# Kernel tuning notes

Hardware: AMD Instinct MI355X
Metric: run time of the kernel (lower is better)

The kernel has to match this reference:

```python
import jax, jax.numpy as jnp
import numpy as np

N, E = 50000, 1600000
IN_CH, OUT_CH = 256, 128
NUM_REL, NUM_BASES = 8, 4


def setup_inputs() -> dict:
    key = jax.random.key(0)
    ks = jax.random.split(key, 9)
    s = 0.05  # small init scale, mimics uniform(size, param)
    return {
        "x": jax.random.normal(ks[0], (N, IN_CH), dtype=jnp.float32),
        "edge_src": jax.random.randint(ks[1], (E,), 0, N, dtype=jnp.int32),
        "edge_dst": jax.random.randint(ks[2], (E,), 0, N, dtype=jnp.int32),
        "edge_type": jax.random.randint(ks[3], (E,), 0, NUM_REL, dtype=jnp.int32),
        "norm": jax.random.uniform(ks[4], (E,), dtype=jnp.float32),
        "basis": jax.random.normal(ks[5], (NUM_BASES, IN_CH, OUT_CH), dtype=jnp.float32) * s,
        "att": jax.random.normal(ks[6], (NUM_REL, NUM_BASES), dtype=jnp.float32) * s,
        "root": jax.random.normal(ks[7], (IN_CH, OUT_CH), dtype=jnp.float32) * s,
        "bias": jax.random.normal(ks[8], (OUT_CH,), dtype=jnp.float32) * s,
    }


def reference(x, edge_src, edge_dst, edge_type, norm, basis, att, root, bias):
    R, B = att.shape
    in_ch, out_ch = root.shape
    n = x.shape[0]
    # w[r] = sum_b att[r,b] * basis[b]  -> [R, in, out]
    w = jnp.matmul(att, basis.reshape(B, -1)).reshape(R, in_ch, out_ch)
    # Per-edge message m_e = (x[src_e] @ w[type_e]) * norm_e.
    # Equivalent dense form: project x by every relation once, then gather per edge.
    h = jnp.einsum("ni,rio->rno", x, w)            # [R, N, out]
    m = h[edge_type, edge_src] * norm[:, None]      # [E, out]
    # sum-reduce messages at destination nodes (zeros for isolated nodes)
    agg = jax.ops.segment_sum(m, edge_dst, num_segments=n)  # [N, out]
    return agg + jnp.matmul(x, root) + bias
```

## Files before the change

### kernel.cpp

```cpp
#include <hip/hip_runtime.h>

#define IN_CH 256
#define OUT_CH 128
#define NUM_REL 8
#define NUM_BASES 4
#define KK 256
#define NSTEP 8

typedef _Float16 f16x8 __attribute__((ext_vector_type(8)));
typedef _Float16 f16x2 __attribute__((ext_vector_type(2)));
typedef float    f32x4 __attribute__((ext_vector_type(4)));
typedef unsigned short u16x8 __attribute__((ext_vector_type(8)));

typedef const __attribute__((address_space(1))) unsigned int* gas_u32p;
typedef __attribute__((address_space(3))) unsigned int*       las_u32p;
#define GLOAD16(g, l) __builtin_amdgcn_global_load_lds( \
    (gas_u32p)(const void*)(g), (las_u32p)(void*)(l), 16, 0, 0)

__device__ __forceinline__ unsigned short f2h(float f) {
    const _Float16 h = (_Float16)f;
    return __builtin_bit_cast(unsigned short, h);
}

__global__ __launch_bounds__(256) void k_build_wT(
    const float* __restrict__ att, const float* __restrict__ basis,
    const float* __restrict__ root, unsigned short* __restrict__ wT)
{
    const int idx = blockIdx.x * 256 + threadIdx.x;
    const int r = idx >> 15, io = idx & 32767;
    const int i = io >> 7, o = io & 127;
    float v;
    if (r < NUM_REL) {
        const int S = IN_CH * OUT_CH;
        v = att[r*4+0]*basis[io] + att[r*4+1]*basis[S+io]
          + att[r*4+2]*basis[2*S+io] + att[r*4+3]*basis[3*S+io];
    } else {
        v = root[io];
    }
    wT[((size_t)r * OUT_CH + o) * KK + i] = f2h(v);
}

__global__ __launch_bounds__(256) void k_cvt_x(
    const float* __restrict__ x, unsigned short* __restrict__ xh, int total4)
{
    const int idx = blockIdx.x * 256 + threadIdx.x;
    if (idx >= total4) return;
    const float4 v = *(const float4*)(x + (size_t)idx * 4);
    ushort4 o;
    o.x = f2h(v.x); o.y = f2h(v.y); o.z = f2h(v.z); o.w = f2h(v.w);
    *(ushort4*)(xh + (size_t)idx * 4) = o;
}

__global__ __launch_bounds__(256) void k_mm(
    const unsigned short* __restrict__ xh,
    const unsigned short* __restrict__ wTb,
    const float* __restrict__ bias,
    float* __restrict__ Df32,
    unsigned short* __restrict__ D16,
    int N, int rootIdx)
{
    const int rr = blockIdx.y;
    const unsigned short* __restrict__ Wt = wTb + (size_t)rr * OUT_CH * KK;
    const int row0 = blockIdx.x * 128;

    __shared__ unsigned short As[2][128 * 32];
    __shared__ unsigned short Bs[2][128 * 32];

    const int tid  = threadIdx.x;
    const int lane = tid & 63;
    const int wv   = tid >> 6;
    const int wr   = wv >> 1;
    const int wc   = wv & 1;
    const int lrow = lane & 15;
    const int q    = lane >> 4;
    const int sw   = (lrow >> 1) & 3;

    f32x4 acc[4][4];
#pragma unroll
    for (int m = 0; m < 4; ++m)
#pragma unroll
        for (int n = 0; n < 4; ++n) acc[m][n] = f32x4{0.f, 0.f, 0.f, 0.f};

    auto STAGE = [&](int b, int s) {
        const int k0 = s * 32;
#pragma unroll
        for (int i = 0; i < 2; ++i) {
            const int c = tid + i * 256;
            const int trow = c >> 2, slot = c & 3;
            const int qsrc = slot ^ ((trow >> 1) & 3);
            int grow = row0 + trow; if (grow >= N) grow = N - 1;
            GLOAD16(xh + (size_t)grow * KK + k0 + qsrc * 8, &As[b][c * 8]);
            GLOAD16(Wt + (size_t)trow * KK + k0 + qsrc * 8, &Bs[b][c * 8]);
        }
    };

    STAGE(0, 0);
    __syncthreads();

#pragma unroll 2
    for (int s = 0; s < NSTEP; ++s) {
        const int cur = s & 1;
        if (s + 1 < NSTEP) STAGE(cur ^ 1, s + 1);

        u16x8 af[4], bg[4];
#pragma unroll
        for (int m = 0; m < 4; ++m)
            af[m] = *(const u16x8*)
                &As[cur][(wr * 64 + m * 16 + lrow) * 32 + ((q ^ sw) * 8)];
#pragma unroll
        for (int n = 0; n < 4; ++n)
            bg[n] = *(const u16x8*)
                &Bs[cur][(wc * 64 + n * 16 + lrow) * 32 + ((q ^ sw) * 8)];
#pragma unroll
        for (int m = 0; m < 4; ++m)
#pragma unroll
            for (int n = 0; n < 4; ++n)
                acc[m][n] = __builtin_amdgcn_mfma_f32_16x16x32_f16(
                    __builtin_bit_cast(f16x8, af[m]),
                    __builtin_bit_cast(f16x8, bg[n]), acc[m][n], 0, 0, 0);

        __syncthreads();
    }

    if (rr == rootIdx) {
        float bv[4];
#pragma unroll
        for (int n = 0; n < 4; ++n) bv[n] = bias[wc * 64 + n * 16 + lrow];
#pragma unroll
        for (int m = 0; m < 4; ++m)
#pragma unroll
            for (int j = 0; j < 4; ++j) {
                const int row = row0 + wr * 64 + m * 16 + q * 4 + j;
                if (row < N) {
#pragma unroll
                    for (int n = 0; n < 4; ++n)
                        Df32[(size_t)row * OUT_CH + wc * 64 + n * 16 + lrow] =
                            acc[m][n][j] + bv[n];
                }
            }
    } else {
        unsigned short* __restrict__ Dh = D16 + (size_t)rr * N * OUT_CH;
#pragma unroll
        for (int m = 0; m < 4; ++m)
#pragma unroll
            for (int j = 0; j < 4; ++j) {
                const int row = row0 + wr * 64 + m * 16 + q * 4 + j;
                if (row < N) {
#pragma unroll
                    for (int n = 0; n < 4; ++n)
                        Dh[(size_t)row * OUT_CH + wc * 64 + n * 16 + lrow] =
                            f2h(acc[m][n][j]);
                }
            }
    }
}

__global__ __launch_bounds__(256) void k_zero(int* __restrict__ p, int n) {
    const int i = blockIdx.x * 256 + threadIdx.x;
    if (i < n) p[i] = 0;
}

__global__ __launch_bounds__(256) void k_hist8(
    const int* __restrict__ edst, const int* __restrict__ etype,
    int* __restrict__ deg8, int E) {
    const int e = blockIdx.x * 256 + threadIdx.x;
    if (e < E) atomicAdd(&deg8[edst[e] * 8 + etype[e]], 1);
}

__global__ __launch_bounds__(256) void k_scan_blk(
    const int* __restrict__ deg, int* __restrict__ oplus1,
    int* __restrict__ btot, int M8)
{
    __shared__ int wsum[4];
    const int tid = threadIdx.x, lane = tid & 63, wv = tid >> 6;
    const int base = blockIdx.x * 1024 + tid * 4;
    int v[4]; int s = 0;
#pragma unroll
    for (int j = 0; j < 4; ++j) {
        v[j] = (base + j < M8) ? deg[base + j] : 0;
        s += v[j];
    }
    int sc = s;
#pragma unroll
    for (int d = 1; d < 64; d <<= 1) {
        const int t = __shfl_up(sc, d);
        if (lane >= d) sc += t;
    }
    if (lane == 63) wsum[wv] = sc;
    __syncthreads();
    int wpre = 0;
#pragma unroll
    for (int j = 0; j < 4; ++j) wpre += (j < wv) ? wsum[j] : 0;
    int run = wpre + sc - s;
#pragma unroll
    for (int j = 0; j < 4; ++j) {
        run += v[j];
        if (base + j < M8) oplus1[base + j] = run;
    }
    if (tid == 255) btot[blockIdx.x] = run;
}

__global__ __launch_bounds__(256) void k_scan_mid(
    const int* __restrict__ btot, int* __restrict__ bbase, int nblk)
{
    __shared__ int sm[512];
    const int tid = threadIdx.x;
    for (int i = tid; i < nblk; i += 256) sm[i] = btot[i];
    __syncthreads();
    if (tid == 0) {
        int run = 0;
        for (int i = 0; i < nblk; ++i) { const int t = sm[i]; sm[i] = run; run += t; }
    }
    __syncthreads();
    for (int i = tid; i < nblk; i += 256) bbase[i] = sm[i];
}

__global__ __launch_bounds__(256) void k_scan_add(
    int* __restrict__ offsets8, int* __restrict__ cursor8,
    const int* __restrict__ bbase, int M8)
{
    const int base = blockIdx.x * 1024 + threadIdx.x * 4;
    const int b = bbase[blockIdx.x];
#pragma unroll
    for (int j = 0; j < 4; ++j) {
        const int i1 = base + j + 1;
        if (base + j < M8) {
            const int v = offsets8[i1] + b;
            offsets8[i1] = v;
            if (i1 < M8) cursor8[i1] = v;
        }
    }
    if (blockIdx.x == 0 && threadIdx.x == 0) {
        offsets8[0] = 0;
        cursor8[0]  = 0;
    }
}

__global__ __launch_bounds__(256) void k_fill8(
    const int* __restrict__ esrc, const int* __restrict__ edst,
    const int* __restrict__ etype, const float* __restrict__ norm,
    int* __restrict__ cursor8, uint2* __restrict__ pedge, int E) {
    const int e = blockIdx.x * 256 + threadIdx.x;
    if (e >= E) return;
    const int t = etype[e];
    const int pos = atomicAdd(&cursor8[edst[e] * 8 + t], 1);
    pedge[pos] = make_uint2((unsigned)(esrc[e] | (t << 27)),
                            __float_as_uint(norm[e]));
}

__global__ __launch_bounds__(256) void k_gather(
    const unsigned short* __restrict__ h,
    const int*   __restrict__ offsets8,
    const uint2* __restrict__ pedge,
    float* __restrict__ out,
    int N, int r0, int r1)
{
    const int wid  = blockIdx.x * 4 + (threadIdx.x >> 6);
    if (wid >= N) return;
    const int lane = threadIdx.x & 63;
    const int s = offsets8[wid * 8 + r0];
    const int e = offsets8[wid * 8 + r1];
    if (e == s) return;
    float2 acc = {0.f, 0.f};
#pragma unroll 4
    for (int p = s; p < e; ++p) {
        const uint2 ed = pedge[p];
        const int key = (int)ed.x;
        const float nm = __uint_as_float(ed.y);
        const int t   = (key >> 27) - r0;
        const int src = key & 0x07FFFFFF;
        const unsigned vp = *(const unsigned*)(
            h + (((size_t)t * N + src) << 7) + lane * 2);
        const f16x2 hv = __builtin_bit_cast(f16x2, vp);
        acc.x = fmaf((float)hv[0], nm, acc.x);
        acc.y = fmaf((float)hv[1], nm, acc.y);
    }
    float* op = out + ((size_t)wid << 7) + lane * 2;
    const float2 cur = *(const float2*)op;
    *(float2*)op = {cur.x + acc.x, cur.y + acc.y};
}

extern "C" void kernel_launch(void* const* d_in, const int* in_sizes, int n_in,
                              void* d_out, int out_size, void* d_ws, size_t ws_size,
                              hipStream_t stream) {
    const float* x     = (const float*)d_in[0];
    const int*   esrc  = (const int*)d_in[1];
    const int*   edst  = (const int*)d_in[2];
    const int*   etype = (const int*)d_in[3];
    const float* norm  = (const float*)d_in[4];
    const float* basis = (const float*)d_in[5];
    const float* att   = (const float*)d_in[6];
    const float* root  = (const float*)d_in[7];
    const float* bias  = (const float*)d_in[8];
    float* out = (float*)d_out;

    const int N  = in_sizes[0] / IN_CH;
    const int E  = in_sizes[1];
    const int M8 = N * 8;
    const int nblkA = (M8 + 1023) / 1024;

    unsigned short* wT = (unsigned short*)d_ws;
    unsigned short* xh = wT + (size_t)9 * OUT_CH * KK;
    int* deg8     = (int*)(xh + (size_t)N * KK);
    int* cursor8  = deg8;
    int* offsets8 = deg8 + M8;
    int* btot     = offsets8 + M8 + 1;
    int* bbase    = btot + nblkA;
    size_t poff = (size_t)((char*)(bbase + nblkA) - (char*)d_ws);
    poff = (poff + 7) & ~(size_t)7;
    uint2* pedge = (uint2*)((char*)d_ws + poff);
    size_t hoff = poff + (size_t)E * 8;
    hoff = (hoff + 255) & ~(size_t)255;
    unsigned short* h = (unsigned short*)((char*)d_ws + hoff);

    const size_t perRel = (size_t)N * OUT_CH * 2;
    int CR;
    {
        const size_t avail = (ws_size > hoff) ? (ws_size - hoff) : 0;
        const size_t fit = avail / perRel;
        if      (fit >= 8) CR = 8;
        else if (fit >= 4) CR = 4;
        else if (fit >= 2) CR = 2;
        else               CR = 1;
    }

    const int nbE  = (E + 255) / 256;
    const int nbM8 = (M8 + 255) / 256;
    const int nbG  = (N + 127) / 128;
    const int gblocks = (N + 3) / 4;

    k_build_wT<<<(9 * IN_CH * OUT_CH) / 256, 256, 0, stream>>>(att, basis, root, wT);
    k_cvt_x<<<(N * IN_CH / 4 + 255) / 256, 256, 0, stream>>>(x, xh, N * IN_CH / 4);

    k_zero<<<nbM8, 256, 0, stream>>>(deg8, M8);
    k_hist8<<<nbE, 256, 0, stream>>>(edst, etype, deg8, E);
    k_scan_blk<<<nblkA, 256, 0, stream>>>(deg8, offsets8 + 1, btot, M8);
    k_scan_mid<<<1, 256, 0, stream>>>(btot, bbase, nblkA);
    k_scan_add<<<nblkA, 256, 0, stream>>>(offsets8, cursor8, bbase, M8);
    k_fill8<<<nbE, 256, 0, stream>>>(esrc, edst, etype, norm, cursor8, pedge, E);

    if (CR >= NUM_REL) {
        k_mm<<<dim3(nbG, NUM_REL + 1), 256, 0, stream>>>(
            xh, wT, bias, out, h, N, NUM_REL);
        k_gather<<<gblocks, 256, 0, stream>>>(
            h, offsets8, pedge, out, N, 0, NUM_REL);
    } else {
        k_mm<<<dim3(nbG, 1), 256, 0, stream>>>(
            xh, wT + (size_t)NUM_REL * OUT_CH * KK, bias, out, h, N, 0);
        for (int rr0 = 0; rr0 < NUM_REL; rr0 += CR) {
            const int cr = (NUM_REL - rr0 < CR) ? (NUM_REL - rr0) : CR;
            k_mm<<<dim3(nbG, cr), 256, 0, stream>>>(
                xh, wT + (size_t)rr0 * OUT_CH * KK, bias, out, h, N, -1);
            k_gather<<<gblocks, 256, 0, stream>>>(
                h, offsets8, pedge, out, N, rr0, rr0 + cr);
        }
    }
}
```

Before: 432.1 us.

## Replace per-(node,relation) CSR build with two-pass bucketed binning by destination

```diff
diff --git a/kernel.cpp b/kernel.cpp
--- a/kernel.cpp
+++ b/kernel.cpp
@@ -6,6 +6,8 @@
 #define NUM_BASES 4
 #define KK 256
 #define NSTEP 8
+#define NBSH 7
+#define EPB 4096
 
 typedef _Float16 f16x8 __attribute__((ext_vector_type(8)));
 typedef _Float16 f16x2 __attribute__((ext_vector_type(2)));
@@ -160,97 +162,116 @@
     if (i < n) p[i] = 0;
 }
 
-__global__ __launch_bounds__(256) void k_hist8(
-    const int* __restrict__ edst, const int* __restrict__ etype,
-    int* __restrict__ deg8, int E) {
-    const int e = blockIdx.x * 256 + threadIdx.x;
-    if (e < E) atomicAdd(&deg8[edst[e] * 8 + etype[e]], 1);
-}
-
-__global__ __launch_bounds__(256) void k_scan_blk(
-    const int* __restrict__ deg, int* __restrict__ oplus1,
-    int* __restrict__ btot, int M8)
-{
-    __shared__ int wsum[4];
-    const int tid = threadIdx.x, lane = tid & 63, wv = tid >> 6;
-    const int base = blockIdx.x * 1024 + tid * 4;
-    int v[4]; int s = 0;
-#pragma unroll
-    for (int j = 0; j < 4; ++j) {
-        v[j] = (base + j < M8) ? deg[base + j] : 0;
-        s += v[j];
-    }
-    int sc = s;
-#pragma unroll
-    for (int d = 1; d < 64; d <<= 1) {
-        const int t = __shfl_up(sc, d);
-        if (lane >= d) sc += t;
-    }
-    if (lane == 63) wsum[wv] = sc;
-    __syncthreads();
-    int wpre = 0;
-#pragma unroll
-    for (int j = 0; j < 4; ++j) wpre += (j < wv) ? wsum[j] : 0;
-    int run = wpre + sc - s;
-#pragma unroll
-    for (int j = 0; j < 4; ++j) {
-        run += v[j];
-        if (base + j < M8) oplus1[base + j] = run;
-    }
-    if (tid == 255) btot[blockIdx.x] = run;
-}
-
-__global__ __launch_bounds__(256) void k_scan_mid(
-    const int* __restrict__ btot, int* __restrict__ bbase, int nblk)
-{
-    __shared__ int sm[512];
+__global__ __launch_bounds__(256) void k_histB(
+    const int* __restrict__ edst, int* __restrict__ bhist, int E, int NB)
+{
+    __shared__ int lh[512];
     const int tid = threadIdx.x;
-    for (int i = tid; i < nblk; i += 256) sm[i] = btot[i];
+    for (int i = tid; i < 512; i += 256) lh[i] = 0;
+    __syncthreads();
+    const int base = blockIdx.x * EPB;
+#pragma unroll
+    for (int k = 0; k < EPB / 256; ++k) {
+        const int e = base + k * 256 + tid;
+        if (e < E) atomicAdd(&lh[edst[e] >> NBSH], 1);
+    }
+    __syncthreads();
+    for (int i = tid; i < NB; i += 256) {
+        const int c = lh[i];
+        if (c) atomicAdd(&bhist[i], c);
+    }
+}
+
+__global__ __launch_bounds__(256) void k_scanB(
+    const int* __restrict__ bhist, int* __restrict__ bucketBase,
+    int* __restrict__ bucketCursor, int NB)
+{
+    __shared__ int sm[513];
+    const int tid = threadIdx.x;
+    for (int i = tid; i < NB; i += 256) sm[i] = bhist[i];
     __syncthreads();
     if (tid == 0) {
         int run = 0;
-        for (int i = 0; i < nblk; ++i) { const int t = sm[i]; sm[i] = run; run += t; }
-    }
-    __syncthreads();
-    for (int i = tid; i < nblk; i += 256) bbase[i] = sm[i];
-}
-
-__global__ __launch_bounds__(256) void k_scan_add(
-    int* __restrict__ offsets8, int* __restrict__ cursor8,
-    const int* __restrict__ bbase, int M8)
-{
-    const int base = blockIdx.x * 1024 + threadIdx.x * 4;
-    const int b = bbase[blockIdx.x];
-#pragma unroll
-    for (int j = 0; j < 4; ++j) {
-        const int i1 = base + j + 1;
-        if (base + j < M8) {
-            const int v = offsets8[i1] + b;
-            offsets8[i1] = v;
-            if (i1 < M8) cursor8[i1] = v;
-        }
-    }
-    if (blockIdx.x == 0 && threadIdx.x == 0) {
-        offsets8[0] = 0;
-        cursor8[0]  = 0;
-    }
-}
-
-__global__ __launch_bounds__(256) void k_fill8(
+        for (int i = 0; i < NB; ++i) { const int t = sm[i]; sm[i] = run; run += t; }
+        sm[NB] = run;
+    }
+    __syncthreads();
+    for (int i = tid; i <= NB; i += 256) bucketBase[i] = sm[i];
+    for (int i = tid; i < NB; i += 256) bucketCursor[i] = sm[i];
+}
+
+__global__ __launch_bounds__(256) void k_binA(
     const int* __restrict__ esrc, const int* __restrict__ edst,
     const int* __restrict__ etype, const float* __restrict__ norm,
-    int* __restrict__ cursor8, uint2* __restrict__ pedge, int E) {
-    const int e = blockIdx.x * 256 + threadIdx.x;
-    if (e >= E) return;
-    const int t = etype[e];
-    const int pos = atomicAdd(&cursor8[edst[e] * 8 + t], 1);
-    pedge[pos] = make_uint2((unsigned)(esrc[e] | (t << 27)),
-                            __float_as_uint(norm[e]));
+    int* __restrict__ bucketCursor, uint2* __restrict__ pedgeA, int E)
+{
+    __shared__ int lh[512], resBase[512], lcur[512];
+    const int tid = threadIdx.x;
+    for (int i = tid; i < 512; i += 256) { lh[i] = 0; lcur[i] = 0; }
+    __syncthreads();
+    const int base = blockIdx.x * EPB;
+    uint2 rec[EPB / 256];
+    int   bkt[EPB / 256];
+#pragma unroll
+    for (int k = 0; k < EPB / 256; ++k) {
+        const int e = base + k * 256 + tid;
+        if (e < E) {
+            const int d = edst[e];
+            bkt[k] = d >> NBSH;
+            rec[k] = make_uint2(
+                (unsigned)(esrc[e] | (etype[e] << 16) | ((d & 127) << 19)),
+                __float_as_uint(norm[e]));
+            atomicAdd(&lh[bkt[k]], 1);
+        } else bkt[k] = -1;
+    }
+    __syncthreads();
+    for (int i = tid; i < 512; i += 256) {
+        const int c = lh[i];
+        if (c) resBase[i] = atomicAdd(&bucketCursor[i], c);
+    }
+    __syncthreads();
+#pragma unroll
+    for (int k = 0; k < EPB / 256; ++k) {
+        if (bkt[k] >= 0) {
+            const int r = atomicAdd(&lcur[bkt[k]], 1);
+            pedgeA[resBase[bkt[k]] + r] = rec[k];
+        }
+    }
+}
+
+__global__ __launch_bounds__(256) void k_binB(
+    const uint2* __restrict__ pedgeA, const int* __restrict__ bucketBase,
+    int* __restrict__ offsetsN, uint2* __restrict__ pedgeB, int N, int E)
+{
+    __shared__ int lh[128], lbase[128], lcur[128];
+    const int tid = threadIdx.x;
+    const int b = blockIdx.x;
+    const int s = bucketBase[b], e = bucketBase[b + 1];
+    if (tid < 128) { lh[tid] = 0; lcur[tid] = 0; }
+    __syncthreads();
+    for (int p = s + tid; p < e; p += 256)
+        atomicAdd(&lh[(pedgeA[p].x >> 19) & 127], 1);
+    __syncthreads();
+    if (tid == 0) {
+        int run = s;
+        for (int j = 0; j < 128; ++j) { const int c = lh[j]; lbase[j] = run; run += c; }
+    }
+    __syncthreads();
+    const int n0 = b << NBSH;
+    if (tid < 128 && n0 + tid < N) offsetsN[n0 + tid] = lbase[tid];
+    if (b == gridDim.x - 1 && tid == 0) offsetsN[N] = E;
+    for (int p = s + tid; p < e; p += 256) {
+        const uint2 r = pedgeA[p];
+        const int j = (r.x >> 19) & 127;
+        const int rk = atomicAdd(&lcur[j], 1);
+        pedgeB[lbase[j] + rk] = make_uint2(
+            (r.x & 0xFFFF) | (((r.x >> 16) & 7) << 27), r.y);
+    }
 }
 
 __global__ __launch_bounds__(256) void k_gather(
     const unsigned short* __restrict__ h,
-    const int*   __restrict__ offsets8,
+    const int*   __restrict__ offsetsN,
     const uint2* __restrict__ pedge,
     float* __restrict__ out,
     int N, int r0, int r1)
@@ -258,19 +279,20 @@
     const int wid  = blockIdx.x * 4 + (threadIdx.x >> 6);
     if (wid >= N) return;
     const int lane = threadIdx.x & 63;
-    const int s = offsets8[wid * 8 + r0];
-    const int e = offsets8[wid * 8 + r1];
+    const int s = offsetsN[wid];
+    const int e = offsetsN[wid + 1];
     if (e == s) return;
     float2 acc = {0.f, 0.f};
 #pragma unroll 4
     for (int p = s; p < e; ++p) {
         const uint2 ed = pedge[p];
         const int key = (int)ed.x;
+        const int t   = key >> 27;
+        if (t < r0 || t >= r1) continue;
         const float nm = __uint_as_float(ed.y);
-        const int t   = (key >> 27) - r0;
         const int src = key & 0x07FFFFFF;
         const unsigned vp = *(const unsigned*)(
-            h + (((size_t)t * N + src) << 7) + lane * 2);
+            h + (((size_t)(t - r0) * N + src) << 7) + lane * 2);
         const f16x2 hv = __builtin_bit_cast(f16x2, vp);
         acc.x = fmaf((float)hv[0], nm, acc.x);
         acc.y = fmaf((float)hv[1], nm, acc.y);
@@ -296,20 +318,20 @@
 
     const int N  = in_sizes[0] / IN_CH;
     const int E  = in_sizes[1];
-    const int M8 = N * 8;
-    const int nblkA = (M8 + 1023) / 1024;
+    const int NB = (N + (1 << NBSH) - 1) >> NBSH;
+    const int nbBin = (E + EPB - 1) / EPB;
 
     unsigned short* wT = (unsigned short*)d_ws;
     unsigned short* xh = wT + (size_t)9 * OUT_CH * KK;
-    int* deg8     = (int*)(xh + (size_t)N * KK);
-    int* cursor8  = deg8;
-    int* offsets8 = deg8 + M8;
-    int* btot     = offsets8 + M8 + 1;
-    int* bbase    = btot + nblkA;
-    size_t poff = (size_t)((char*)(bbase + nblkA) - (char*)d_ws);
+    int* bhist        = (int*)(xh + (size_t)N * KK);
+    int* bucketBase   = bhist + NB;
+    int* bucketCursor = bucketBase + NB + 1;
+    int* offsetsN     = bucketCursor + NB;
+    size_t poff = (size_t)((char*)(offsetsN + N + 1) - (char*)d_ws);
     poff = (poff + 7) & ~(size_t)7;
-    uint2* pedge = (uint2*)((char*)d_ws + poff);
-    size_t hoff = poff + (size_t)E * 8;
+    uint2* pedgeA = (uint2*)((char*)d_ws + poff);
+    uint2* pedgeB = pedgeA + E;
+    size_t hoff = poff + (size_t)E * 16;
     hoff = (hoff + 255) & ~(size_t)255;
     unsigned short* h = (unsigned short*)((char*)d_ws + hoff);
 
@@ -324,26 +346,24 @@
         else               CR = 1;
     }
 
-    const int nbE  = (E + 255) / 256;
-    const int nbM8 = (M8 + 255) / 256;
-    const int nbG  = (N + 127) / 128;
+    const int nbG = (N + 127) / 128;
     const int gblocks = (N + 3) / 4;
 
     k_build_wT<<<(9 * IN_CH * OUT_CH) / 256, 256, 0, stream>>>(att, basis, root, wT);
     k_cvt_x<<<(N * IN_CH / 4 + 255) / 256, 256, 0, stream>>>(x, xh, N * IN_CH / 4);
 
-    k_zero<<<nbM8, 256, 0, stream>>>(deg8, M8);
-    k_hist8<<<nbE, 256, 0, stream>>>(edst, etype, deg8, E);
-    k_scan_blk<<<nblkA, 256, 0, stream>>>(deg8, offsets8 + 1, btot, M8);
-    k_scan_mid<<<1, 256, 0, stream>>>(btot, bbase, nblkA);
-    k_scan_add<<<nblkA, 256, 0, stream>>>(offsets8, cursor8, bbase, M8);
-    k_fill8<<<nbE, 256, 0, stream>>>(esrc, edst, etype, norm, cursor8, pedge, E);
+    k_zero<<<(NB + 255) / 256, 256, 0, stream>>>(bhist, NB);
+    k_histB<<<nbBin, 256, 0, stream>>>(edst, bhist, E, NB);
+    k_scanB<<<1, 256, 0, stream>>>(bhist, bucketBase, bucketCursor, NB);
+    k_binA<<<nbBin, 256, 0, stream>>>(esrc, edst, etype, norm,
+                                      bucketCursor, pedgeA, E);
+    k_binB<<<NB, 256, 0, stream>>>(pedgeA, bucketBase, offsetsN, pedgeB, N, E);
 
     if (CR >= NUM_REL) {
         k_mm<<<dim3(nbG, NUM_REL + 1), 256, 0, stream>>>(
             xh, wT, bias, out, h, N, NUM_REL);
         k_gather<<<gblocks, 256, 0, stream>>>(
-            h, offsets8, pedge, out, N, 0, NUM_REL);
+            h, offsetsN, pedgeB, out, N, 0, NUM_REL);
     } else {
         k_mm<<<dim3(nbG, 1), 256, 0, stream>>>(
             xh, wT + (size_t)NUM_REL * OUT_CH * KK, bias, out, h, N, 0);
@@ -352,7 +372,7 @@
             k_mm<<<dim3(nbG, cr), 256, 0, stream>>>(
                 xh, wT + (size_t)rr0 * OUT_CH * KK, bias, out, h, N, -1);
             k_gather<<<gblocks, 256, 0, stream>>>(
-                h, offsets8, pedge, out, N, rr0, rr0 + cr);
+                h, offsetsN, pedgeB, out, N, rr0, rr0 + cr);
         }
     }
 }
```

Measured after the change: 409.9 us. 1.05x faster.
